# Optimization experiments

Measured on AMD Instinct MI355X. Metric: run time of the kernel, lower is better.

Reference implementation:

```python
import jax, jax.numpy as jnp
import numpy as np
import math

IN_DIM = 1024
INTER_DIM = 1024
HIDDEN_DIM = 1024
OUT_DIM = 1024
NUM_GROUPS = 16
N = 8192
EPS = 1e-5


def setup_inputs() -> dict:
    key = jax.random.key(0)
    ks = jax.random.split(key, 20)
    def lin(kw, kb, fan_out, fan_in):
        bound = 1.0 / math.sqrt(fan_in)
        W = jax.random.uniform(kw, (fan_out, fan_in), jnp.float32, -bound, bound)
        b = jax.random.uniform(kb, (fan_out,), jnp.float32, -bound, bound)
        return W, b
    Wq, bq = lin(ks[0], ks[1], INTER_DIM, IN_DIM)
    Wk, bk = lin(ks[2], ks[3], INTER_DIM, IN_DIM)
    Wv, bv = lin(ks[4], ks[5], INTER_DIM, IN_DIM)
    Wr, br = lin(ks[6], ks[7], HIDDEN_DIM, INTER_DIM)
    Wc, bc = lin(ks[8], ks[9], HIDDEN_DIM, OUT_DIM)
    Wp, bp = lin(ks[10], ks[11], OUT_DIM, 2 * HIDDEN_DIM)
    return {
        'h': jax.random.normal(ks[12], (N, IN_DIM), jnp.float32),
        'D': jax.random.uniform(ks[13], (N, N), jnp.float32),
        'h_prime': jax.random.normal(ks[14], (N, OUT_DIM), jnp.float32),
        'Wq': Wq, 'bq': bq, 'Wk': Wk, 'bk': bk, 'Wv': Wv, 'bv': bv,
        'Wr': Wr, 'br': br, 'Wc': Wc, 'bc': bc, 'Wp': Wp, 'bp': bp,
        'prelu_w': jnp.full((OUT_DIM,), 0.25, jnp.float32),
        'gn_w': jnp.ones((OUT_DIM,), jnp.float32),
        'gn_b': jnp.zeros((OUT_DIM,), jnp.float32),
    }


def reference(h, D, h_prime, Wq, bq, Wk, bk, Wv, bv, Wr, br, Wc, bc, Wp, bp, prelu_w, gn_w, gn_b):
    # projections [N, inter]
    Q = h @ Wq.T + bq
    K = h @ Wk.T + bk
    V = h @ Wv.T + bv
    # decay-masked retention: softmax(D * QK^T / sqrt(d)) @ V
    scores = (Q @ K.T) * (1.0 / math.sqrt(INTER_DIM))   # [N, N]
    attn = jax.nn.softmax(D * scores, axis=-1)
    h_ret = attn @ V                                     # [N, inter]
    h_ret = jax.nn.gelu(h_ret @ Wr.T + br, approximate=False)  # [N, hidden]
    h_cat = h_prime @ Wc.T + bc                          # [N, hidden]
    combined = jnp.concatenate([h_ret, h_cat], axis=-1)  # [N, 2*hidden]
    x = combined @ Wp.T + bp                             # [N, out]
    # PReLU (per-channel slope over feature dim)
    x = jnp.where(x >= 0, x, prelu_w[None, :] * x)
    # GroupNorm over (C, N) layout: normalize each group of channels jointly over all N
    xt = x.T                                             # [C, N]
    xg = xt.reshape(NUM_GROUPS, -1)                      # [G, (C/G)*N]
    mean = jnp.mean(xg, axis=1, keepdims=True)
    var = jnp.var(xg, axis=1, keepdims=True)
    xg = (xg - mean) * jax.lax.rsqrt(var + EPS)
    xt = xg.reshape(OUT_DIM, N) * gn_w[:, None] + gn_b[:, None]
    return xt.T                                          # [N, out]
```

## Files before the change

### kernel.cpp

```cpp
#include <hip/hip_runtime.h>
#include <hip/hip_bf16.h>


typedef __bf16 bf16x8 __attribute__((ext_vector_type(8)));
typedef float f32x4 __attribute__((ext_vector_type(4)));
typedef unsigned short ushort_t;


__device__ __forceinline__ void gload_lds16(const void* g, void* lds) {
  __builtin_amdgcn_global_load_lds((const __attribute__((address_space(1))) void*)g,
                                   (__attribute__((address_space(3))) void*)lds,
                                   16, 0, 0);
}

__device__ __forceinline__ ushort_t f2bu(float x) {
  __hip_bfloat16 h = __float2bfloat16(x);
  return *reinterpret_cast<ushort_t*>(&h);
}

#define FENCE() asm volatile("" ::: "memory")
#define BARRIER() do { FENCE(); __builtin_amdgcn_s_barrier(); FENCE(); } while (0)


__global__ void f2b_kernel(const float* __restrict__ s, __hip_bfloat16* __restrict__ d, int n) {
  const int i4 = (blockIdx.x * 256 + threadIdx.x) * 4;
  if (i4 >= n) return;
  const float4 v = *(const float4*)(s + i4);
  ushort4 o;
  o.x = f2bu(v.x); o.y = f2bu(v.y); o.z = f2bu(v.z); o.w = f2bu(v.w);
  *(ushort4*)((ushort_t*)d + i4) = o;
}

template <int EPI>
__global__ __launch_bounds__(512, 2)
void g8(const __hip_bfloat16* __restrict__ A, const __hip_bfloat16* __restrict__ B,
        __hip_bfloat16* __restrict__ Cb, float* __restrict__ Cf,
        int K, int ldc, int nbnLog2,
        const float* __restrict__ biasN, const float* __restrict__ biasM,
        const float* __restrict__ rowsum, const float* __restrict__ prelu_w,
        float* __restrict__ gstats) {
  __shared__ __align__(16) char ldsm[98304];
  const int tid = threadIdx.x, w = tid >> 6, l = tid & 63;
  const int wm = w >> 2, wn = w & 3;

  const int orig = blockIdx.x;
  const int wg = (orig & 7) * 32 + (orig >> 3);
  const int bm = wg >> nbnLog2, bn = wg & ((1 << nbnLog2) - 1);

  const size_t rowB = (size_t)K * 2;
  const char* Ag = (const char*)A + (size_t)bm * 128 * rowB;
  const char* Bg = (const char*)B + (size_t)bn * 256 * rowB;
  const int NT = K >> 6;

  auto stageU = [&](int p, int unit, const char* srcbase) {
    char* ldsu = ldsm + p * 49152 + unit * 16384;
#pragma unroll
    for (int i = 0; i < 2; ++i) {
      const int cb = i * 512 + w * 64;
      const int c = cb + l;
      const int r = c >> 3;
      const int j = (c & 7) ^ (r & 7);
      gload_lds16(srcbase + (size_t)r * rowB + j * 16, ldsu + cb * 16);
    }
  };
  auto stA = [&](int p, int kt) { stageU(p, 0, Ag + (size_t)kt * 128); };
  auto stB = [&](int p, int hh, int kt) {
    stageU(p, 1 + hh, Bg + (size_t)hh * 128 * rowB + (size_t)kt * 128);
  };

  auto rdA = [&](int p, int f, int kk) -> bf16x8 {
    const int R = wm * 64 + f * 16 + (l & 15);
    const int j = kk * 4 + (l >> 4);
    const int chunk = R * 8 + (j ^ (R & 7));
    return *(const bf16x8*)(ldsm + p * 49152 + chunk * 16);
  };
  auto rdB = [&](int p, int nf, int kk) -> bf16x8 {
    const int Rg = wn * 64 + nf * 16 + (l & 15);
    const int hh = Rg >> 7, Rl = Rg & 127;
    const int j = kk * 4 + (l >> 4);
    const int chunk = Rl * 8 + (j ^ (Rl & 7));
    return *(const bf16x8*)(ldsm + p * 49152 + 16384 + hh * 16384 + chunk * 16);
  };

  stA(0, 0); stB(0, 0, 0); stB(0, 1, 0);
  stA(1, 1);
  asm volatile("s_waitcnt vmcnt(2)" ::: "memory");
  BARRIER();

  f32x4 acc[4][4] = {};
  bf16x8 Af[4][2], Bf[2][2];

#define PH_A_B01(p)                                            \
  _Pragma("unroll") for (int f = 0; f < 4; ++f)                \
  _Pragma("unroll") for (int kk = 0; kk < 2; ++kk)             \
      Af[f][kk] = rdA(p, f, kk);                               \
  _Pragma("unroll") for (int g = 0; g < 2; ++g)                \
  _Pragma("unroll") for (int kk = 0; kk < 2; ++kk)             \
      Bf[g][kk] = rdB(p, g, kk)

#define PH_B23(p)                                              \
  _Pragma("unroll") for (int g = 0; g < 2; ++g)                \
  _Pragma("unroll") for (int kk = 0; kk < 2; ++kk)             \
      Bf[g][kk] = rdB(p, 2 + g, kk)

#define PRE_MFMA()                                             \
  asm volatile("s_waitcnt lgkmcnt(0)" ::: "memory");           \
  __builtin_amdgcn_sched_barrier(0)

#define MF(CB)                                                          \
  __builtin_amdgcn_s_setprio(1);                                        \
  _Pragma("unroll") for (int f = 0; f < 4; ++f)                         \
  _Pragma("unroll") for (int g = 0; g < 2; ++g)                         \
  _Pragma("unroll") for (int kk = 0; kk < 2; ++kk)                      \
      acc[f][(CB) + g] = __builtin_amdgcn_mfma_f32_16x16x32_bf16(       \
          Af[f][kk], Bf[g][kk], acc[f][(CB) + g], 0, 0, 0);             \
  __builtin_amdgcn_s_setprio(0)

#pragma unroll 1
  for (int t = 0; t < NT; t += 2) {
    const bool s2 = (t + 2 < NT);
    PH_A_B01(0);
    stB(1, 0, t + 1); stB(1, 1, t + 1);
    BARRIER(); PRE_MFMA();
    MF(0);
    BARRIER();
    PH_B23(0);
    if (s2) stA(0, t + 2);
    if (s2) asm volatile("s_waitcnt vmcnt(2)" ::: "memory");
    else    asm volatile("s_waitcnt vmcnt(0)" ::: "memory");
    BARRIER(); PRE_MFMA();
    MF(2);
    BARRIER();
    PH_A_B01(1);
    if (s2) { stB(0, 0, t + 2); stB(0, 1, t + 2); }
    BARRIER(); PRE_MFMA();
    MF(0);
    BARRIER();
    PH_B23(1);
    if (s2) {
      stA(1, t + 3);
      asm volatile("s_waitcnt vmcnt(2)" ::: "memory");
    }
    BARRIER(); PRE_MFMA();
    MF(2);
    BARRIER();
  }
#undef PH_A_B01
#undef PH_B23
#undef PRE_MFMA
#undef MF

  const int r0 = bm * 128 + wm * 64, c0 = bn * 256 + wn * 64;
  float gs = 0.f, gq = 0.f;
#pragma unroll
  for (int mf = 0; mf < 4; ++mf) {
#pragma unroll
    for (int i = 0; i < 4; ++i) {
      const int row = r0 + mf * 16 + ((l >> 4) << 2) + i;
      float rscale = 1.0f;
      if (EPI == 3) rscale = 1.0f / rowsum[row];
#pragma unroll
      for (int nf = 0; nf < 4; ++nf) {
        const int col = c0 + nf * 16 + (l & 15);
        float v = acc[mf][nf][i];
        if (EPI == 0) {
          v += biasN[col];
        } else if (EPI == 1) {
          v += biasM[row];
        } else if (EPI == 3) {
          v = v * rscale + biasN[col];
          v = 0.5f * v * (1.0f + erff(v * 0.70710678118654752f));
        } else if (EPI == 4) {
          v += biasN[col];
          v = (v >= 0.f) ? v : prelu_w[col] * v;
        }
        if (EPI == 4) {
          Cf[(size_t)row * ldc + col] = v;
          gs += v; gq += v * v;
        } else {
          Cb[(size_t)row * ldc + col] = __float2bfloat16(v);
        }
      }
    }
  }
  if (EPI == 4) {
#pragma unroll
    for (int m = 1; m < 64; m <<= 1) {
      gs += __shfl_xor(gs, m);
      gq += __shfl_xor(gq, m);
    }
    if (l == 0) {
      const int g = c0 >> 6;
      atomicAdd(&gstats[g * 2 + 0], gs);
      atomicAdd(&gstats[g * 2 + 1], gq);
    }
  }
}

__global__ __launch_bounds__(512, 2)
void pkern8(const __hip_bfloat16* __restrict__ Q, const __hip_bfloat16* __restrict__ Kmat,
            const float* __restrict__ D, __hip_bfloat16* __restrict__ P,
            float* __restrict__ rowsum, int nt) {
  __shared__ __align__(16) char ldsm[131072];
  const int tid = threadIdx.x, w = tid >> 6, l = tid & 63;
  const int wm = w >> 2, wn = w & 3;

  const int orig = blockIdx.x;
  const int wg = (orig & 7) * 128 + (orig >> 3);
  const int bm = wg >> 5, bn = wg & 31;

  const char* Ag = (const char*)Q + (size_t)bm * 256 * 2048;
  const char* Bg = (const char*)Kmat + (size_t)bn * 256 * 2048;

  auto stage = [&](int p, int ab, int hh, int kt) {
    const char* srcbase = (ab ? Bg : Ag) + (size_t)hh * 128 * 2048 + (size_t)kt * 128;
    char* ldsbase = ldsm + p * 65536 + ab * 32768 + hh * 16384;
#pragma unroll
    for (int i = 0; i < 2; ++i) {
      const int cbase = i * 512 + w * 64;
      const int c = cbase + l;
      const int r = c >> 3;
      const int j = (c & 7) ^ (r & 7);
      gload_lds16(srcbase + (size_t)r * 2048 + j * 16, ldsbase + cbase * 16);
    }
  };

  auto rdA = [&](int p, int mh, int kk, int f) -> bf16x8 {
    const int R = mh * 64 + f * 16 + (l & 15);
    const int j = kk * 4 + (l >> 4);
    const int chunk = R * 8 + (j ^ (R & 7));
    return *(const bf16x8*)(ldsm + p * 65536 + wm * 16384 + chunk * 16);
  };
  auto rdB = [&](int p, int nh, int kk, int g) -> bf16x8 {
    const int R = (wn & 1) * 64 + (nh * 2 + g) * 16 + (l & 15);
    const int j = kk * 4 + (l >> 4);
    const int chunk = R * 8 + (j ^ (R & 7));
    return *(const bf16x8*)(ldsm + p * 65536 + 32768 + (wn >> 1) * 16384 + chunk * 16);
  };

  stage(0, 0, 0, 0); stage(0, 0, 1, 0); stage(0, 1, 0, 0); stage(0, 1, 1, 0);
  stage(1, 1, 0, 1); stage(1, 0, 0, 1); stage(1, 0, 1, 1);
  asm volatile("s_waitcnt vmcnt(6)" ::: "memory");
  BARRIER();

  f32x4 acc[8][4] = {};
  bf16x8 Af[4][2], B0[2][2], B1[2][2];

#define MFMA_QUAD(RB, CB, BREG)                                                          \
  __builtin_amdgcn_s_setprio(1);                                                         \
  _Pragma("unroll") for (int f = 0; f < 4; ++f)                                          \
  _Pragma("unroll") for (int g = 0; g < 2; ++g)                                          \
  _Pragma("unroll") for (int kk = 0; kk < 2; ++kk)                                       \
      acc[(RB) + f][(CB) + g] = __builtin_amdgcn_mfma_f32_16x16x32_bf16(                 \
          Af[f][kk], BREG[g][kk], acc[(RB) + f][(CB) + g], 0, 0, 0);                     \
  __builtin_amdgcn_s_setprio(0)

#define PRE_MFMA()                                           \
  asm volatile("s_waitcnt lgkmcnt(0)" ::: "memory");         \
  __builtin_amdgcn_sched_barrier(0)

#define RD_A(p, mh)                                          \
  _Pragma("unroll") for (int f = 0; f < 4; ++f)              \
  _Pragma("unroll") for (int kk = 0; kk < 2; ++kk)           \
      Af[f][kk] = rdA(p, mh, kk, f)

#define RD_B(p, nh, DST)                                     \
  _Pragma("unroll") for (int g = 0; g < 2; ++g)              \
  _Pragma("unroll") for (int kk = 0; kk < 2; ++kk)           \
      DST[g][kk] = rdB(p, nh, kk, g)

#pragma unroll 1
  for (int t = 0; t < nt; t += 2) {
    const bool s2 = (t + 2 < nt), s3 = (t + 3 < nt);
    RD_A(0, 0); RD_B(0, 0, B0);
    stage(1, 1, 1, t + 1);
    BARRIER(); PRE_MFMA();
    MFMA_QUAD(0, 0, B0);
    BARRIER();

    RD_B(0, 1, B1);
    BARRIER(); PRE_MFMA();
    MFMA_QUAD(0, 2, B1);
    BARRIER();

    RD_A(0, 1);
    if (s2) stage(0, 1, 0, t + 2);
    BARRIER(); PRE_MFMA();
    MFMA_QUAD(4, 2, B1);
    BARRIER();

    if (s2) stage(0, 0, 0, t + 2);
    if (s2) asm volatile("s_waitcnt vmcnt(4)" ::: "memory");
    else    asm volatile("s_waitcnt vmcnt(0)" ::: "memory");
    BARRIER(); PRE_MFMA();
    MFMA_QUAD(4, 0, B0);
    BARRIER();

    RD_A(1, 0); RD_B(1, 0, B0);
    if (s2) stage(0, 0, 1, t + 2);
    BARRIER(); PRE_MFMA();
    MFMA_QUAD(0, 0, B0);
    BARRIER();

    RD_B(1, 1, B1);
    if (s2) stage(0, 1, 1, t + 2);
    BARRIER(); PRE_MFMA();
    MFMA_QUAD(0, 2, B1);
    BARRIER();

    RD_A(1, 1);
    if (s3) stage(1, 1, 0, t + 3);
    BARRIER(); PRE_MFMA();
    MFMA_QUAD(4, 2, B1);
    BARRIER();

    if (s3) { stage(1, 0, 0, t + 3); stage(1, 0, 1, t + 3); }
    asm volatile("s_waitcnt vmcnt(6)" ::: "memory");
    BARRIER(); PRE_MFMA();
    MFMA_QUAD(4, 0, B0);
    BARRIER();
  }
#undef MFMA_QUAD
#undef PRE_MFMA
#undef RD_A
#undef RD_B

  const int rbase = bm * 256 + wm * 128;
  const int cbase = bn * 256 + wn * 64;
#pragma unroll
  for (int mf = 0; mf < 8; ++mf) {
#pragma unroll
    for (int i = 0; i < 4; ++i) {
      const int row = rbase + mf * 16 + ((l >> 4) << 2) + i;
      float rs = 0.f;
#pragma unroll
      for (int nf = 0; nf < 4; ++nf) {
        const int col = cbase + nf * 16 + (l & 15);
        const float d = D[(size_t)row * 8192 + col];
        const float pv = __expf(d * (acc[mf][nf][i] * 0.03125f));
        P[(size_t)row * 8192 + col] = __float2bfloat16(pv);
        rs += pv;
      }
      rs += __shfl_xor(rs, 1); rs += __shfl_xor(rs, 2);
      rs += __shfl_xor(rs, 4); rs += __shfl_xor(rs, 8);
      if ((l & 15) == 0) atomicAdd(&rowsum[row], rs);
    }
  }
}


__global__ void gn_finalize(const float* __restrict__ x, const float* __restrict__ gstats,
                            const float* __restrict__ gw, const float* __restrict__ gb,
                            float* __restrict__ out, int n) {
  __shared__ float sm[16], sr[16];
  if (threadIdx.x < 16) {
    const float cnt = 64.0f * 8192.0f;
    const float s = gstats[threadIdx.x * 2 + 0];
    const float q = gstats[threadIdx.x * 2 + 1];
    const float mean = s / cnt;
    const float var = q / cnt - mean * mean;
    sm[threadIdx.x] = mean;
    sr[threadIdx.x] = rsqrtf(var + 1e-5f);
  }
  __syncthreads();
  const int i4 = (blockIdx.x * 256 + threadIdx.x) * 4;
  if (i4 >= n) return;
  const float4 v = *(const float4*)(x + i4);
  const int c = i4 & 1023;
  const int g = c >> 6;
  const float mean = sm[g], r = sr[g];
  float4 o;
  o.x = (v.x - mean) * r * gw[c + 0] + gb[c + 0];
  o.y = (v.y - mean) * r * gw[c + 1] + gb[c + 1];
  o.z = (v.z - mean) * r * gw[c + 2] + gb[c + 2];
  o.w = (v.w - mean) * r * gw[c + 3] + gb[c + 3];
  *(float4*)(out + i4) = o;
}


extern "C" void kernel_launch(void* const* d_in, const int* in_sizes, int n_in,
                              void* d_out, int out_size, void* d_ws, size_t ws_size,
                              hipStream_t stream) {
  const float* h  = (const float*)d_in[0];
  const float* D  = (const float*)d_in[1];
  const float* hp = (const float*)d_in[2];
  const float* Wq = (const float*)d_in[3];
  const float* bq = (const float*)d_in[4];
  const float* Wk = (const float*)d_in[5];
  const float* bk = (const float*)d_in[6];
  const float* Wv = (const float*)d_in[7];
  const float* bv = (const float*)d_in[8];
  const float* Wr = (const float*)d_in[9];
  const float* br = (const float*)d_in[10];
  const float* Wc = (const float*)d_in[11];
  const float* bc = (const float*)d_in[12];
  const float* Wp = (const float*)d_in[13];
  const float* bp = (const float*)d_in[14];
  const float* pw = (const float*)d_in[15];
  const float* gw = (const float*)d_in[16];
  const float* gb = (const float*)d_in[17];
  float* out = (float*)d_out;

  char* ws = (char*)d_ws;
  size_t off = 0;
  auto alloc = [&](size_t b) {
    char* p = ws + off;
    off += (b + 255) & ~(size_t)255;
    return p;
  };
  __hip_bfloat16* hb   = (__hip_bfloat16*)alloc(8192ull * 1024 * 2);
  __hip_bfloat16* hpb  = (__hip_bfloat16*)alloc(8192ull * 1024 * 2);
  __hip_bfloat16* Wqb  = (__hip_bfloat16*)alloc(1024ull * 1024 * 2);
  __hip_bfloat16* Wkb  = (__hip_bfloat16*)alloc(1024ull * 1024 * 2);
  __hip_bfloat16* Wvb  = (__hip_bfloat16*)alloc(1024ull * 1024 * 2);
  __hip_bfloat16* Wrb  = (__hip_bfloat16*)alloc(1024ull * 1024 * 2);
  __hip_bfloat16* Wcb  = (__hip_bfloat16*)alloc(1024ull * 1024 * 2);
  __hip_bfloat16* Wpb  = (__hip_bfloat16*)alloc(1024ull * 2048 * 2);
  __hip_bfloat16* Qb   = (__hip_bfloat16*)alloc(8192ull * 1024 * 2);
  __hip_bfloat16* Kb   = (__hip_bfloat16*)alloc(8192ull * 1024 * 2);
  __hip_bfloat16* Vt   = (__hip_bfloat16*)alloc(1024ull * 8192 * 2);
  __hip_bfloat16* R0   = (__hip_bfloat16*)alloc(8192ull * 1024 * 2);
  __hip_bfloat16* comb = (__hip_bfloat16*)alloc(8192ull * 2048 * 2);
  __hip_bfloat16* P    = (__hip_bfloat16*)alloc(8192ull * 8192 * 2);
  float* xbuf   = (float*)alloc(8192ull * 1024 * 4);
  float* rowsum = (float*)alloc(8192ull * 4);
  float* gstats = (float*)alloc(128);
  if (off > ws_size) return;

  hipMemsetAsync(rowsum, 0, 8192 * 4, stream);
  hipMemsetAsync(gstats, 0, 128, stream);

  auto cvt = [&](const float* s, __hip_bfloat16* d, int n) {
    f2b_kernel<<<dim3((n / 4 + 255) / 256), dim3(256), 0, stream>>>(s, d, n);
  };
  cvt(h, hb, 8192 * 1024);
  cvt(hp, hpb, 8192 * 1024);
  cvt(Wq, Wqb, 1024 * 1024);
  cvt(Wk, Wkb, 1024 * 1024);
  cvt(Wv, Wvb, 1024 * 1024);
  cvt(Wr, Wrb, 1024 * 1024);
  cvt(Wc, Wcb, 1024 * 1024);
  cvt(Wp, Wpb, 1024 * 2048);

  g8<0><<<dim3(256), 512, 0, stream>>>(hb, Wqb, Qb, nullptr, 1024, 1024, 2, bq, nullptr, nullptr, nullptr, nullptr);
  g8<0><<<dim3(256), 512, 0, stream>>>(hb, Wkb, Kb, nullptr, 1024, 1024, 2, bk, nullptr, nullptr, nullptr, nullptr);
  g8<1><<<dim3(256), 512, 0, stream>>>(Wvb, hb, Vt, nullptr, 1024, 8192, 5, nullptr, bv, nullptr, nullptr, nullptr);
  pkern8<<<dim3(1024), 512, 0, stream>>>(Qb, Kb, D, P, rowsum, 16);
  g8<2><<<dim3(256), 512, 0, stream>>>(P, Vt, R0, nullptr, 8192, 1024, 2, nullptr, nullptr, nullptr, nullptr, nullptr);
  g8<3><<<dim3(256), 512, 0, stream>>>(R0, Wrb, comb, nullptr, 1024, 2048, 2, br, nullptr, rowsum, nullptr, nullptr);
  g8<0><<<dim3(256), 512, 0, stream>>>(hpb, Wcb, comb + 1024, nullptr, 1024, 2048, 2, bc, nullptr, nullptr, nullptr, nullptr);
  g8<4><<<dim3(256), 512, 0, stream>>>(comb, Wpb, nullptr, xbuf, 2048, 1024, 2, bp, nullptr, nullptr, pw, gstats);
  gn_finalize<<<dim3(8192), 256, 0, stream>>>(xbuf, gstats, gw, gb, out, 8192 * 1024);
}
```

Baseline: 656.2 us.

## Shrink QK^T score kernel tile and stage epilogue through LDS for coalesced access

Replaces the 256x256-tile, 512-thread score/exp kernel with a 128x128-tile, 256-thread variant using half the LDS, launched on 4096 blocks. The epilogue now stages accumulators through padded LDS so each thread reads D with float4 loads and writes eight bf16 values per store, and the row-sum reduction needs fewer shuffles and atomics. The MFMA loop order is also changed to iterate k outermost. The intent is better occupancy and coalesced D/P traffic in this memory-heavy stage, at the cost of less operand reuse per tile and more Q/K reloads from global memory.

New measurement: 637.9 us. -2.8%, faster.

```diff
diff --git a/kernel.cpp b/kernel.cpp
--- a/kernel.cpp
+++ b/kernel.cpp
@@ -5,6 +5,7 @@
 typedef __bf16 bf16x8 __attribute__((ext_vector_type(8)));
 typedef float f32x4 __attribute__((ext_vector_type(4)));
 typedef unsigned short ushort_t;
+typedef unsigned short ushort8 __attribute__((ext_vector_type(8)));
 
 
 __device__ __forceinline__ void gload_lds16(const void* g, void* lds) {
@@ -109,9 +110,9 @@
 
 #define MF(CB)                                                          \
   __builtin_amdgcn_s_setprio(1);                                        \
+  _Pragma("unroll") for (int kk = 0; kk < 2; ++kk)                      \
   _Pragma("unroll") for (int f = 0; f < 4; ++f)                         \
   _Pragma("unroll") for (int g = 0; g < 2; ++g)                         \
-  _Pragma("unroll") for (int kk = 0; kk < 2; ++kk)                      \
       acc[f][(CB) + g] = __builtin_amdgcn_mfma_f32_16x16x32_bf16(       \
           Af[f][kk], Bf[g][kk], acc[f][(CB) + g], 0, 0, 0);             \
   __builtin_amdgcn_s_setprio(0)
@@ -197,156 +198,172 @@
   }
 }
 
-__global__ __launch_bounds__(512, 2)
-void pkern8(const __hip_bfloat16* __restrict__ Q, const __hip_bfloat16* __restrict__ Kmat,
+#define EPAD2 132
+__global__ __launch_bounds__(256, 2)
+void pkern2(const __hip_bfloat16* __restrict__ Q, const __hip_bfloat16* __restrict__ Kmat,
             const float* __restrict__ D, __hip_bfloat16* __restrict__ P,
             float* __restrict__ rowsum, int nt) {
-  __shared__ __align__(16) char ldsm[131072];
+  __shared__ __align__(16) char ldsm[65536];
   const int tid = threadIdx.x, w = tid >> 6, l = tid & 63;
-  const int wm = w >> 2, wn = w & 3;
+  const int wm = w >> 1, wn = w & 1;
 
   const int orig = blockIdx.x;
-  const int wg = (orig & 7) * 128 + (orig >> 3);
-  const int bm = wg >> 5, bn = wg & 31;
-
-  const char* Ag = (const char*)Q + (size_t)bm * 256 * 2048;
-  const char* Bg = (const char*)Kmat + (size_t)bn * 256 * 2048;
-
-  auto stage = [&](int p, int ab, int hh, int kt) {
-    const char* srcbase = (ab ? Bg : Ag) + (size_t)hh * 128 * 2048 + (size_t)kt * 128;
-    char* ldsbase = ldsm + p * 65536 + ab * 32768 + hh * 16384;
-#pragma unroll
-    for (int i = 0; i < 2; ++i) {
-      const int cbase = i * 512 + w * 64;
-      const int c = cbase + l;
+  const int wg = (orig & 7) * 512 + (orig >> 3);
+  const int bm = wg >> 6, bn = wg & 63;
+
+  const char* Ag = (const char*)Q + (size_t)bm * 128 * 2048;
+  const char* Bg = (const char*)Kmat + (size_t)bn * 128 * 2048;
+
+  auto stageU = [&](int p, int unit, const char* srcbase) {
+    char* ldsu = ldsm + p * 32768 + unit * 16384;
+#pragma unroll
+    for (int i = 0; i < 4; ++i) {
+      const int cb = i * 256 + w * 64;
+      const int c = cb + l;
       const int r = c >> 3;
       const int j = (c & 7) ^ (r & 7);
-      gload_lds16(srcbase + (size_t)r * 2048 + j * 16, ldsbase + cbase * 16);
-    }
-  };
-
-  auto rdA = [&](int p, int mh, int kk, int f) -> bf16x8 {
-    const int R = mh * 64 + f * 16 + (l & 15);
+      gload_lds16(srcbase + (size_t)r * 2048 + j * 16, ldsu + cb * 16);
+    }
+  };
+  auto stA = [&](int p, int kt) { stageU(p, 0, Ag + (size_t)kt * 128); };
+  auto stB = [&](int p, int kt) { stageU(p, 1, Bg + (size_t)kt * 128); };
+
+  auto rdA = [&](int p, int f, int kk) -> bf16x8 {
+    const int R = wm * 64 + f * 16 + (l & 15);
     const int j = kk * 4 + (l >> 4);
     const int chunk = R * 8 + (j ^ (R & 7));
-    return *(const bf16x8*)(ldsm + p * 65536 + wm * 16384 + chunk * 16);
-  };
-  auto rdB = [&](int p, int nh, int kk, int g) -> bf16x8 {
-    const int R = (wn & 1) * 64 + (nh * 2 + g) * 16 + (l & 15);
+    return *(const bf16x8*)(ldsm + p * 32768 + chunk * 16);
+  };
+  auto rdB = [&](int p, int nf, int kk) -> bf16x8 {
+    const int R = wn * 64 + nf * 16 + (l & 15);
     const int j = kk * 4 + (l >> 4);
     const int chunk = R * 8 + (j ^ (R & 7));
-    return *(const bf16x8*)(ldsm + p * 65536 + 32768 + (wn >> 1) * 16384 + chunk * 16);
-  };
-
-  stage(0, 0, 0, 0); stage(0, 0, 1, 0); stage(0, 1, 0, 0); stage(0, 1, 1, 0);
-  stage(1, 1, 0, 1); stage(1, 0, 0, 1); stage(1, 0, 1, 1);
-  asm volatile("s_waitcnt vmcnt(6)" ::: "memory");
+    return *(const bf16x8*)(ldsm + p * 32768 + 16384 + chunk * 16);
+  };
+
+  stA(0, 0); stB(0, 0);
+  stA(1, 1);
+  asm volatile("s_waitcnt vmcnt(4)" ::: "memory");
   BARRIER();
 
-  f32x4 acc[8][4] = {};
-  bf16x8 Af[4][2], B0[2][2], B1[2][2];
-
-#define MFMA_QUAD(RB, CB, BREG)                                                          \
-  __builtin_amdgcn_s_setprio(1);                                                         \
-  _Pragma("unroll") for (int f = 0; f < 4; ++f)                                          \
-  _Pragma("unroll") for (int g = 0; g < 2; ++g)                                          \
-  _Pragma("unroll") for (int kk = 0; kk < 2; ++kk)                                       \
-      acc[(RB) + f][(CB) + g] = __builtin_amdgcn_mfma_f32_16x16x32_bf16(                 \
-          Af[f][kk], BREG[g][kk], acc[(RB) + f][(CB) + g], 0, 0, 0);                     \
+  f32x4 acc[4][4] = {};
+  bf16x8 Af[4][2], Bf[2][2];
+
+#define PH_A_B01(p)                                            \
+  _Pragma("unroll") for (int f = 0; f < 4; ++f)                \
+  _Pragma("unroll") for (int kk = 0; kk < 2; ++kk)             \
+      Af[f][kk] = rdA(p, f, kk);                               \
+  _Pragma("unroll") for (int g = 0; g < 2; ++g)                \
+  _Pragma("unroll") for (int kk = 0; kk < 2; ++kk)             \
+      Bf[g][kk] = rdB(p, g, kk)
+
+#define PH_B23(p)                                              \
+  _Pragma("unroll") for (int g = 0; g < 2; ++g)                \
+  _Pragma("unroll") for (int kk = 0; kk < 2; ++kk)             \
+      Bf[g][kk] = rdB(p, 2 + g, kk)
+
+#define PRE_MFMA()                                             \
+  asm volatile("s_waitcnt lgkmcnt(0)" ::: "memory");           \
+  __builtin_amdgcn_sched_barrier(0)
+
+#define MF(CB)                                                          \
+  __builtin_amdgcn_s_setprio(1);                                        \
+  _Pragma("unroll") for (int kk = 0; kk < 2; ++kk)                      \
+  _Pragma("unroll") for (int f = 0; f < 4; ++f)                         \
+  _Pragma("unroll") for (int g = 0; g < 2; ++g)                         \
+      acc[f][(CB) + g] = __builtin_amdgcn_mfma_f32_16x16x32_bf16(       \
+          Af[f][kk], Bf[g][kk], acc[f][(CB) + g], 0, 0, 0);             \
   __builtin_amdgcn_s_setprio(0)
-
-#define PRE_MFMA()                                           \
-  asm volatile("s_waitcnt lgkmcnt(0)" ::: "memory");         \
-  __builtin_amdgcn_sched_barrier(0)
-
-#define RD_A(p, mh)                                          \
-  _Pragma("unroll") for (int f = 0; f < 4; ++f)              \
-  _Pragma("unroll") for (int kk = 0; kk < 2; ++kk)           \
-      Af[f][kk] = rdA(p, mh, kk, f)
-
-#define RD_B(p, nh, DST)                                     \
-  _Pragma("unroll") for (int g = 0; g < 2; ++g)              \
-  _Pragma("unroll") for (int kk = 0; kk < 2; ++kk)           \
-      DST[g][kk] = rdB(p, nh, kk, g)
 
 #pragma unroll 1
   for (int t = 0; t < nt; t += 2) {
     const bool s2 = (t + 2 < nt), s3 = (t + 3 < nt);
-    RD_A(0, 0); RD_B(0, 0, B0);
-    stage(1, 1, 1, t + 1);
-    BARRIER(); PRE_MFMA();
-    MFMA_QUAD(0, 0, B0);
-    BARRIER();
-
-    RD_B(0, 1, B1);
-    BARRIER(); PRE_MFMA();
-    MFMA_QUAD(0, 2, B1);
-    BARRIER();
-
-    RD_A(0, 1);
-    if (s2) stage(0, 1, 0, t + 2);
-    BARRIER(); PRE_MFMA();
-    MFMA_QUAD(4, 2, B1);
-    BARRIER();
-
-    if (s2) stage(0, 0, 0, t + 2);
+    PH_A_B01(0);
+    stB(1, t + 1);
+    BARRIER(); PRE_MFMA();
+    MF(0);
+    BARRIER();
+    PH_B23(0);
+    if (s2) stA(0, t + 2);
     if (s2) asm volatile("s_waitcnt vmcnt(4)" ::: "memory");
     else    asm volatile("s_waitcnt vmcnt(0)" ::: "memory");
     BARRIER(); PRE_MFMA();
-    MFMA_QUAD(4, 0, B0);
-    BARRIER();
-
-    RD_A(1, 0); RD_B(1, 0, B0);
-    if (s2) stage(0, 0, 1, t + 2);
-    BARRIER(); PRE_MFMA();
-    MFMA_QUAD(0, 0, B0);
-    BARRIER();
-
-    RD_B(1, 1, B1);
-    if (s2) stage(0, 1, 1, t + 2);
-    BARRIER(); PRE_MFMA();
-    MFMA_QUAD(0, 2, B1);
-    BARRIER();
-
-    RD_A(1, 1);
-    if (s3) stage(1, 1, 0, t + 3);
-    BARRIER(); PRE_MFMA();
-    MFMA_QUAD(4, 2, B1);
-    BARRIER();
-
-    if (s3) { stage(1, 0, 0, t + 3); stage(1, 0, 1, t + 3); }
-    asm volatile("s_waitcnt vmcnt(6)" ::: "memory");
-    BARRIER(); PRE_MFMA();
-    MFMA_QUAD(4, 0, B0);
-    BARRIER();
-  }
-#undef MFMA_QUAD
+    MF(2);
+    BARRIER();
+    PH_A_B01(1);
+    if (s2) stB(0, t + 2);
+    BARRIER(); PRE_MFMA();
+    MF(0);
+    BARRIER();
+    PH_B23(1);
+    if (s3) stA(1, t + 3);
+    if (s3)      asm volatile("s_waitcnt vmcnt(4)" ::: "memory");
+    else if (s2) asm volatile("s_waitcnt vmcnt(0)" ::: "memory");
+    else         asm volatile("s_waitcnt vmcnt(0)" ::: "memory");
+    BARRIER(); PRE_MFMA();
+    MF(2);
+    BARRIER();
+  }
+#undef PH_A_B01
+#undef PH_B23
 #undef PRE_MFMA
-#undef RD_A
-#undef RD_B
-
-  const int rbase = bm * 256 + wm * 128;
-  const int cbase = bn * 256 + wn * 64;
-#pragma unroll
-  for (int mf = 0; mf < 8; ++mf) {
-#pragma unroll
-    for (int i = 0; i < 4; ++i) {
-      const int row = rbase + mf * 16 + ((l >> 4) << 2) + i;
+#undef MF
+
+  float* lds32 = (float*)ldsm;
+  const int rbase = bm * 128, cbase = bn * 128;
+  const int rth = tid >> 3;
+  const int cl = (tid & 7) * 16;
+#pragma unroll 1
+  for (int h = 0; h < 2; ++h) {
+    float4 dreg[8];
+#pragma unroll
+    for (int it = 0; it < 2; ++it) {
+      const size_t gof = (size_t)(rbase + h * 64 + it * 32 + rth) * 8192 + (cbase + cl);
+#pragma unroll
+      for (int q = 0; q < 4; ++q) dreg[it * 4 + q] = *(const float4*)(D + gof + q * 4);
+    }
+    BARRIER();
+    if (wm == h) {
+#pragma unroll
+      for (int mf = 0; mf < 4; ++mf)
+#pragma unroll
+        for (int nf = 0; nf < 4; ++nf)
+#pragma unroll
+          for (int i = 0; i < 4; ++i)
+            lds32[(mf * 16 + ((l >> 4) << 2) + i) * EPAD2 + (wn * 64 + nf * 16 + (l & 15))] =
+                acc[mf][nf][i];
+    }
+    asm volatile("s_waitcnt lgkmcnt(0)" ::: "memory");
+    BARRIER();
+#pragma unroll
+    for (int it = 0; it < 2; ++it) {
+      const int rl = it * 32 + rth;
+      const int row = rbase + h * 64 + rl;
+      const size_t gof = (size_t)row * 8192 + (cbase + cl);
+      float pv[16];
+#pragma unroll
+      for (int q = 0; q < 4; ++q) {
+        const float4 s = *(const float4*)(lds32 + rl * EPAD2 + cl + q * 4);
+        const float4 d = dreg[it * 4 + q];
+        pv[q * 4 + 0] = __expf(d.x * (s.x * 0.03125f));
+        pv[q * 4 + 1] = __expf(d.y * (s.y * 0.03125f));
+        pv[q * 4 + 2] = __expf(d.z * (s.z * 0.03125f));
+        pv[q * 4 + 3] = __expf(d.w * (s.w * 0.03125f));
+      }
+      ushort8 o0, o1;
+#pragma unroll
+      for (int q = 0; q < 8; ++q) { o0[q] = f2bu(pv[q]); o1[q] = f2bu(pv[8 + q]); }
+      *(ushort8*)((ushort_t*)P + gof) = o0;
+      *(ushort8*)((ushort_t*)P + gof + 8) = o1;
       float rs = 0.f;
 #pragma unroll
-      for (int nf = 0; nf < 4; ++nf) {
-        const int col = cbase + nf * 16 + (l & 15);
-        const float d = D[(size_t)row * 8192 + col];
-        const float pv = __expf(d * (acc[mf][nf][i] * 0.03125f));
-        P[(size_t)row * 8192 + col] = __float2bfloat16(pv);
-        rs += pv;
-      }
-      rs += __shfl_xor(rs, 1); rs += __shfl_xor(rs, 2);
-      rs += __shfl_xor(rs, 4); rs += __shfl_xor(rs, 8);
-      if ((l & 15) == 0) atomicAdd(&rowsum[row], rs);
-    }
-  }
-}
+      for (int q = 0; q < 16; ++q) rs += pv[q];
+      rs += __shfl_xor(rs, 1); rs += __shfl_xor(rs, 2); rs += __shfl_xor(rs, 4);
+      if ((tid & 7) == 0) atomicAdd(&rowsum[row], rs);
+    }
+  }
+}
+#undef EPAD2
 
 
 __global__ void gn_finalize(const float* __restrict__ x, const float* __restrict__ gstats,
@@ -445,7 +462,7 @@
   g8<0><<<dim3(256), 512, 0, stream>>>(hb, Wqb, Qb, nullptr, 1024, 1024, 2, bq, nullptr, nullptr, nullptr, nullptr);
   g8<0><<<dim3(256), 512, 0, stream>>>(hb, Wkb, Kb, nullptr, 1024, 1024, 2, bk, nullptr, nullptr, nullptr, nullptr);
   g8<1><<<dim3(256), 512, 0, stream>>>(Wvb, hb, Vt, nullptr, 1024, 8192, 5, nullptr, bv, nullptr, nullptr, nullptr);
-  pkern8<<<dim3(1024), 512, 0, stream>>>(Qb, Kb, D, P, rowsum, 16);
+  pkern2<<<dim3(4096), 256, 0, stream>>>(Qb, Kb, D, P, rowsum, 16);
   g8<2><<<dim3(256), 512, 0, stream>>>(P, Vt, R0, nullptr, 8192, 1024, 2, nullptr, nullptr, nullptr, nullptr, nullptr);
   g8<3><<<dim3(256), 512, 0, stream>>>(R0, Wrb, comb, nullptr, 1024, 2048, 2, br, nullptr, rowsum, nullptr, nullptr);
   g8<0><<<dim3(256), 512, 0, stream>>>(hpb, Wcb, comb + 1024, nullptr, 1024, 2048, 2, bc, nullptr, nullptr, nullptr, nullptr);
```
